# Kernel tuning notes

Hardware: AMD Instinct MI355X
Metric: run time of the kernel (lower is better)

Reference implementation:

```python
import jax, jax.numpy as jnp
import numpy as np

B, S, E, H = 4, 2048, 1024, 16
HD = E // H  # 64 head dim


def setup_inputs() -> dict:
    key = jax.random.key(0)
    ks = jax.random.split(key, 6)
    x = jax.random.normal(ks[0], (B, S, E), dtype=jnp.float32)
    mask = jax.random.randint(ks[1], (B, S, S), 0, 2, dtype=jnp.int32)
    # per-head qkv Linear(E -> 3*HD), stacked over heads: weight [H, 3*HD, E]
    lim = 1.0 / np.sqrt(E)
    Wqkv = jax.random.uniform(ks[2], (H, 3 * HD, E), minval=-lim, maxval=lim, dtype=jnp.float32)
    bqkv = jax.random.uniform(ks[3], (H, 3 * HD), minval=-lim, maxval=lim, dtype=jnp.float32)
    Wo = jax.random.uniform(ks[4], (E, E), minval=-lim, maxval=lim, dtype=jnp.float32)
    bo = jax.random.uniform(ks[5], (E,), minval=-lim, maxval=lim, dtype=jnp.float32)
    return {"x": x, "mask": mask, "Wqkv": Wqkv, "bqkv": bqkv, "Wo": Wo, "bo": bo}


def reference(x, mask, Wqkv, bqkv, Wo, bo):
    # fused per-head qkv projection: [B,S,E] x [H,3HD,E] -> [B,H,S,3HD]
    qkv = jnp.einsum('bse,hfe->bhsf', x, Wqkv) + bqkv[None, :, None, :]
    q, k, v = jnp.split(qkv, 3, axis=-1)  # each [B,H,S,HD]
    scale = 1.0 / jnp.sqrt(jnp.float32(HD))
    scores = jnp.einsum('bhqd,bhkd->bhqk', q, k) * scale  # [B,H,S,S]
    # NOTE: original masked_fill sets masked scores to 0.0 (not -inf)
    scores = jnp.where(mask[:, None, :, :] == 1, 0.0, scores)
    attn = jax.nn.softmax(scores, axis=-1)
    ctx = jnp.einsum('bhqk,bhkd->bhqd', attn, v)  # [B,H,S,HD]
    ctx = ctx.transpose(0, 2, 1, 3).reshape(B, S, E)  # concat heads
    return ctx @ Wo.T + bo
```

## Files before the change

kernel.cpp:

```cpp
#include <hip/hip_runtime.h>
#include <stdint.h>

#define B_ 4
#define S_ 2048
#define E_ 1024
#define H_ 16
#define HD_ 64

typedef __attribute__((ext_vector_type(8))) short bf16x8;
typedef __attribute__((ext_vector_type(4))) float f32x4;

__device__ __forceinline__ ushort f2b(float f) {
    union { float f; uint32_t u; } c; c.f = f;
    return (ushort)((c.u + 0x8000u) >> 16);
}

__device__ __forceinline__ void gl2lds16(const ushort* g, const ushort* l) {
    __builtin_amdgcn_global_load_lds(
        (const __attribute__((address_space(1))) unsigned int*)g,
        (__attribute__((address_space(3))) unsigned int*)l,
        16, 0, 0);
}
__device__ __forceinline__ void gl2lds16raw(const void* g, const void* l) {
    __builtin_amdgcn_global_load_lds(
        (const __attribute__((address_space(1))) unsigned int*)g,
        (__attribute__((address_space(3))) unsigned int*)l,
        16, 0, 0);
}

__global__ __launch_bounds__(256) void cvt_bf16(const float* __restrict__ src,
                                                ushort* __restrict__ dst, int n4) {
    int i = blockIdx.x * 256 + threadIdx.x;
    if (i < n4) {
        float4 f = ((const float4*)src)[i];
        ushort4 o;
        o.x = f2b(f.x); o.y = f2b(f.y); o.z = f2b(f.z); o.w = f2b(f.w);
        ((ushort4*)dst)[i] = o;
    }
}

__global__ __launch_bounds__(256) void pack_mask(const int* __restrict__ mask,
                                                 uint32_t* __restrict__ mb) {
    int i = blockIdx.x * 256 + threadIdx.x;
    unsigned long long bal = __ballot(mask[i] == 1);
    int lane = threadIdx.x & 63;
    if (lane < 2) {
        int b = i >> 22, q = (i >> 11) & 2047, c = i & 2047;
        int kt = c >> 6;
        mb[((uint64_t)(b * 32 + kt) * 2048 + q) * 2 + lane] =
            (lane == 0) ? (uint32_t)bal : (uint32_t)(bal >> 32);
    }
}

template <int KD>
__device__ __forceinline__ void gemm_bt_core(
    const ushort* __restrict__ A, const ushort* __restrict__ Bm,
    int m0, int n0, ushort* As, ushort* Bs, f32x4 (&acc)[4][4])
{
    const int tid  = threadIdx.x;
    const int lane = tid & 63;
    const int wave = tid >> 6;
    const int wm = wave >> 1, wn = wave & 1;
    const int fr = lane & 15;
    const int fk = (lane >> 4) * 8;
    const int lrow = lane >> 2;
    const int lk   = (lane & 3) * 8;

    const f32x4 fz = {0.f, 0.f, 0.f, 0.f};
#pragma unroll
    for (int i = 0; i < 4; ++i)
#pragma unroll
        for (int j = 0; j < 4; ++j) acc[i][j] = fz;

    for (int kt = 0; kt < KD / 32; ++kt) {
        const int k0 = kt * 32;
        __syncthreads();
#pragma unroll
        for (int t = 0; t < 2; ++t) {
            const int r0 = t * 64 + wave * 16;
            gl2lds16(&A [(uint64_t)(m0 + r0 + lrow) * KD + k0 + lk], &As[r0 * 32]);
            gl2lds16(&Bm[(uint64_t)(n0 + r0 + lrow) * KD + k0 + lk], &Bs[r0 * 32]);
        }
        __syncthreads();
        bf16x8 af[4], bfr[4];
#pragma unroll
        for (int i = 0; i < 4; ++i)
            af[i] = *(const bf16x8*)&As[(wm * 64 + i * 16 + fr) * 32 + fk];
#pragma unroll
        for (int j = 0; j < 4; ++j)
            bfr[j] = *(const bf16x8*)&Bs[(wn * 64 + j * 16 + fr) * 32 + fk];
#pragma unroll
        for (int i = 0; i < 4; ++i)
#pragma unroll
            for (int j = 0; j < 4; ++j)
                acc[i][j] = __builtin_amdgcn_mfma_f32_16x16x32_bf16(af[i], bfr[j], acc[i][j], 0, 0, 0);
    }
}

__global__ __launch_bounds__(256) void qkv_gemm(
    const ushort* __restrict__ xb, const ushort* __restrict__ wb,
    const float* __restrict__ bqkv,
    ushort* __restrict__ qo, ushort* __restrict__ ko, ushort* __restrict__ vto)
{
    __shared__ ushort As[128 * 32];
    __shared__ ushort Bs[128 * 32];
    f32x4 acc[4][4];
    const int i = blockIdx.x;
    const int c = i & 7, t = i >> 3;
    const int n0 = (c + 8 * (t % 3)) * 128;
    const int m0 = (t / 3) * 128;
    gemm_bt_core<1024>(xb, wb, m0, n0, As, Bs, acc);

    const int lane = threadIdx.x & 63, wave = threadIdx.x >> 6;
    const int wm = wave >> 1, wn = wave & 1;
    const int col = lane & 15, rg = lane >> 4;
#pragma unroll
    for (int j = 0; j < 4; ++j) {
        const int n = n0 + wn * 64 + j * 16 + col;
        const int h = n / 192, f = n % 192;
        const float bias = bqkv[n];
#pragma unroll
        for (int i2 = 0; i2 < 4; ++i2) {
            const int mbase = m0 + wm * 64 + i2 * 16 + rg * 4;
            if (f < 128) {
#pragma unroll
                for (int v = 0; v < 4; ++v) {
                    const int m = mbase + v;
                    const int b = m >> 11, s = m & 2047;
                    const float val = acc[i2][j][v] + bias;
                    if (f < 64) qo[((uint64_t)(b * 16 + h) * 2048 + s) * 64 + f]        = f2b(val * 0.125f);
                    else        ko[((uint64_t)(b * 16 + h) * 2048 + s) * 64 + (f - 64)] = f2b(val);
                }
            } else {
                const int b = mbase >> 11, s = mbase & 2047;
                ushort4 pk;
                pk.x = f2b(acc[i2][j][0] + bias);
                pk.y = f2b(acc[i2][j][1] + bias);
                pk.z = f2b(acc[i2][j][2] + bias);
                pk.w = f2b(acc[i2][j][3] + bias);
                *(ushort4*)&vto[((uint64_t)(b * 16 + h) * 64 + (f - 128)) * 2048 + s] = pk;
            }
        }
    }
}

__global__ __launch_bounds__(256, 3) void attn_kernel(
    const ushort* __restrict__ qa, const ushort* __restrict__ ka,
    const ushort* __restrict__ vta, const uint32_t* __restrict__ mbits,
    ushort* __restrict__ ctxo)
{
    __shared__ __align__(16) ushort SMEM[128 * 64];
    __shared__ __align__(16) ushort Ks[2][64 * 64];
    __shared__ __align__(16) ushort Vts[2][64 * 64];
    __shared__ __align__(16) uint32_t Ms[2][256];

    const int bid = blockIdx.x;
    const int qb = bid & 15;
    const int bh = bid >> 4;
    const int b = bh >> 4;
    const int tid = threadIdx.x, lane = tid & 63, wave = tid >> 6;
    const int col = lane & 15, rg = lane >> 4;

    const uint64_t bhoff = (uint64_t)bh * (S_ * 64);
    const ushort* qp = qa + bhoff + (uint64_t)qb * 128 * 64;
    const ushort* kp = ka + bhoff;
    const ushort* vp = vta + bhoff;
    const uint32_t* mkb = mbits + ((uint64_t)(b * 32) * 2048 + qb * 128) * 2;

#pragma unroll
    for (int t4 = 0; t4 < 4; ++t4) {
        const int o = (wave * 4 + t4) * 512;
        gl2lds16(&qp[o + lane * 8], &SMEM[o]);
    }
#pragma unroll
    for (int t = 0; t < 2; ++t) {
        const int o = (wave * 2 + t) * 512;
        gl2lds16(&kp[o + lane * 8], &Ks[0][o]);
        const int r0 = (wave * 2 + t) * 8;
        gl2lds16(&vp[(uint64_t)(r0 + (lane >> 3)) * S_ + (lane & 7) * 8], &Vts[0][r0 * 64]);
    }
    if (wave == 0) gl2lds16raw(mkb + lane * 4, &Ms[0][0]);
    __syncthreads();

    bf16x8 aq[2][2];
#pragma unroll
    for (int i = 0; i < 2; ++i)
#pragma unroll
        for (int k2 = 0; k2 < 2; ++k2)
            aq[i][k2] = *(const bf16x8*)&SMEM[(wave * 32 + i * 16 + col) * 64 + k2 * 32 + rg * 8];

    const f32x4 fz = {0.f, 0.f, 0.f, 0.f};
    f32x4 acc[4][2];
#pragma unroll
    for (int dt = 0; dt < 4; ++dt)
#pragma unroll
        for (int i = 0; i < 2; ++i) acc[dt][i] = fz;
    float lsum[2] = {0.f, 0.f};

    ushort* Ps = &SMEM[wave * 2048];

    for (int kt = 0; kt < 32; ++kt) {
        const int buf = kt & 1;
        if (kt < 31) {
            const uint64_t knext = (uint64_t)(kt + 1) * 4096;
#pragma unroll
            for (int t = 0; t < 2; ++t) {
                const int o = (wave * 2 + t) * 512;
                gl2lds16(&kp[knext + o + lane * 8], &Ks[buf ^ 1][o]);
                const int r0 = (wave * 2 + t) * 8;
                gl2lds16(&vp[(uint64_t)(r0 + (lane >> 3)) * S_ + (kt + 1) * 64 + (lane & 7) * 8],
                         &Vts[buf ^ 1][r0 * 64]);
            }
            if (wave == 0) gl2lds16raw(mkb + (uint64_t)(kt + 1) * 4096 + lane * 4,
                                       &Ms[buf ^ 1][0]);
        }

        f32x4 sc[2][4];
#pragma unroll
        for (int j = 0; j < 4; ++j) {
            bf16x8 bk0 = *(const bf16x8*)&Ks[buf][(j * 16 + col) * 64 + rg * 8];
            bf16x8 bk1 = *(const bf16x8*)&Ks[buf][(j * 16 + col) * 64 + 32 + rg * 8];
#pragma unroll
            for (int i = 0; i < 2; ++i) {
                f32x4 z = __builtin_amdgcn_mfma_f32_16x16x32_bf16(bk0, aq[i][0], fz, 0, 0, 0);
                sc[i][j] = __builtin_amdgcn_mfma_f32_16x16x32_bf16(bk1, aq[i][1], z, 0, 0, 0);
            }
        }

#pragma unroll
        for (int i = 0; i < 2; ++i) {
            const int qrow = i * 16 + col;
            const uint2 mw = *(const uint2*)&Ms[buf][(wave * 32 + qrow) * 2];
            float ts = 0.f;
#pragma unroll
            for (int j = 0; j < 4; ++j) {
                const uint32_t w = (j & 2) ? mw.y : mw.x;
                const int base = (j & 1) * 16 + rg * 4;
                ushort4 pk;
                {
                    const float s0 = ((w >> (base + 0)) & 1u) ? 0.f : sc[i][j][0];
                    const float s1 = ((w >> (base + 1)) & 1u) ? 0.f : sc[i][j][1];
                    const float s2 = ((w >> (base + 2)) & 1u) ? 0.f : sc[i][j][2];
                    const float s3 = ((w >> (base + 3)) & 1u) ? 0.f : sc[i][j][3];
                    const float p0 = __expf(s0), p1 = __expf(s1);
                    const float p2 = __expf(s2), p3 = __expf(s3);
                    ts += (p0 + p1) + (p2 + p3);
                    pk.x = f2b(p0); pk.y = f2b(p1); pk.z = f2b(p2); pk.w = f2b(p3);
                }
                const int u = ((j * 2 + (rg >> 1)) ^ (col & 7));
                *(ushort4*)&Ps[qrow * 64 + u * 8 + (rg & 1) * 4] = pk;
            }
            lsum[i] += ts;
        }

        bf16x8 bp[2][2];
#pragma unroll
        for (int i = 0; i < 2; ++i)
#pragma unroll
            for (int k2 = 0; k2 < 2; ++k2)
                bp[i][k2] = *(const bf16x8*)&Ps[(i * 16 + col) * 64 + (((k2 * 4 + rg) ^ (col & 7)) << 3)];
#pragma unroll
        for (int dt = 0; dt < 4; ++dt) {
            bf16x8 av0 = *(const bf16x8*)&Vts[buf][(dt * 16 + col) * 64 + rg * 8];
            bf16x8 av1 = *(const bf16x8*)&Vts[buf][(dt * 16 + col) * 64 + 32 + rg * 8];
#pragma unroll
            for (int i = 0; i < 2; ++i) {
                acc[dt][i] = __builtin_amdgcn_mfma_f32_16x16x32_bf16(av0, bp[i][0], acc[dt][i], 0, 0, 0);
                acc[dt][i] = __builtin_amdgcn_mfma_f32_16x16x32_bf16(av1, bp[i][1], acc[dt][i], 0, 0, 0);
            }
        }
        __syncthreads();
    }

    float linv[2];
#pragma unroll
    for (int i = 0; i < 2; ++i) {
        float ts = lsum[i];
        ts += __shfl_xor(ts, 16);
        ts += __shfl_xor(ts, 32);
        linv[i] = 1.0f / ts;
    }

#pragma unroll
    for (int dt = 0; dt < 4; ++dt)
#pragma unroll
        for (int i = 0; i < 2; ++i) {
            const int q = wave * 32 + i * 16 + col;
            const int d = dt * 16 + rg * 4;
            const int gg = (d >> 3) ^ (q & 7);
            ushort4 pk;
            pk.x = f2b(acc[dt][i][0] * linv[i]);
            pk.y = f2b(acc[dt][i][1] * linv[i]);
            pk.z = f2b(acc[dt][i][2] * linv[i]);
            pk.w = f2b(acc[dt][i][3] * linv[i]);
            *(ushort4*)&SMEM[q * 64 + gg * 8 + (d & 7)] = pk;
        }
    __syncthreads();
    const int h = bh & 15;
    const uint64_t obase = (uint64_t)(b * S_ + qb * 128) * E_ + (uint64_t)h * 64;
#pragma unroll
    for (int t4 = 0; t4 < 4; ++t4) {
        const int id = tid + t4 * 256;
        const int r = id >> 3, c8 = id & 7;
        *(bf16x8*)&ctxo[obase + (uint64_t)r * E_ + c8 * 8] =
            *(const bf16x8*)&SMEM[r * 64 + ((c8 ^ (r & 7)) << 3)];
    }
}

__global__ __launch_bounds__(256) void out_gemm(
    const ushort* __restrict__ ctxb, const ushort* __restrict__ wob,
    const float* __restrict__ bo, float* __restrict__ out)
{
    __shared__ ushort As[128 * 32];
    __shared__ ushort Bs[128 * 32];
    f32x4 acc[4][4];
    const int i = blockIdx.x;
    const int n0 = (i & 7) * 128;
    const int m0 = (i >> 3) * 128;
    gemm_bt_core<1024>(ctxb, wob, m0, n0, As, Bs, acc);

    const int lane = threadIdx.x & 63, wave = threadIdx.x >> 6;
    const int wm = wave >> 1, wn = wave & 1;
    const int col = lane & 15, rg = lane >> 4;
#pragma unroll
    for (int j = 0; j < 4; ++j) {
        const int n = n0 + wn * 64 + j * 16 + col;
        const float bias = bo[n];
#pragma unroll
        for (int i2 = 0; i2 < 4; ++i2) {
            const int mb2 = m0 + wm * 64 + i2 * 16 + rg * 4;
#pragma unroll
            for (int v = 0; v < 4; ++v)
                out[(uint64_t)(mb2 + v) * 1024 + n] = acc[i2][j][v] + bias;
        }
    }
}

extern "C" void kernel_launch(void* const* d_in, const int* in_sizes, int n_in,
                              void* d_out, int out_size, void* d_ws, size_t ws_size,
                              hipStream_t stream)
{
    const float* x    = (const float*)d_in[0];
    const int*   mask = (const int*)d_in[1];
    const float* Wqkv = (const float*)d_in[2];
    const float* bqkv = (const float*)d_in[3];
    const float* Wo   = (const float*)d_in[4];
    const float* bo   = (const float*)d_in[5];
    float* out = (float*)d_out;

    char* p = (char*)d_ws;
    ushort* xb  = (ushort*)p; p += (size_t)8388608 * 2;
    ushort* wqb = (ushort*)p; p += (size_t)3145728 * 2;
    ushort* wob = (ushort*)p; p += (size_t)1048576 * 2;
    ushort* qo  = (ushort*)p; p += (size_t)8388608 * 2;
    ushort* ko  = (ushort*)p; p += (size_t)8388608 * 2;
    ushort* vto = (ushort*)p; p += (size_t)8388608 * 2;
    ushort* ctx = (ushort*)p; p += (size_t)8388608 * 2;
    uint32_t* mb = (uint32_t*)p;

    cvt_bf16<<<8192, 256, 0, stream>>>(x, xb, 2097152);
    cvt_bf16<<<3072, 256, 0, stream>>>(Wqkv, wqb, 786432);
    cvt_bf16<<<1024, 256, 0, stream>>>(Wo, wob, 262144);
    pack_mask<<<65536, 256, 0, stream>>>(mask, mb);
    qkv_gemm<<<1536, 256, 0, stream>>>(xb, wqb, bqkv, qo, ko, vto);
    attn_kernel<<<1024, 256, 0, stream>>>(qo, ko, vto, mb, ctx);
    out_gemm<<<512, 256, 0, stream>>>(ctx, wob, bo, out);
}
```

Baseline: 405.1 us.

## Keep softmax P in registers via permuted K/V LDS layout; change GEMM grid order

The attention kernel now loads K rows into LDS in a permuted order and with an XOR swizzle on K and V tiles. This lets each lane's score MFMA output line up with the B-operand layout of the PV MFMA, so the exponentiated probabilities are packed straight into registers instead of going through an LDS write and read. It also swaps the two GEMMs to a 2D grid with M-major block order. That changes L2 reuse of weight versus activation tiles and could hurt locality compared with the previous grouped ordering.

```diff
diff --git a/kernel.cpp b/kernel.cpp
--- a/kernel.cpp
+++ b/kernel.cpp
@@ -105,10 +105,8 @@
     __shared__ ushort As[128 * 32];
     __shared__ ushort Bs[128 * 32];
     f32x4 acc[4][4];
-    const int i = blockIdx.x;
-    const int c = i & 7, t = i >> 3;
-    const int n0 = (c + 8 * (t % 3)) * 128;
-    const int m0 = (t / 3) * 128;
+    const int m0 = blockIdx.x * 128;
+    const int n0 = blockIdx.y * 128;
     gemm_bt_core<1024>(xb, wb, m0, n0, As, Bs, acc);
 
     const int lane = threadIdx.x & 63, wave = threadIdx.x >> 6;
@@ -167,18 +165,28 @@
     const ushort* vp = vta + bhoff;
     const uint32_t* mkb = mbits + ((uint64_t)(b * 32) * 2048 + qb * 128) * 2;
 
+    const int lr = lane >> 3;
+    const int usw = (lane & 7) ^ lr;
+    const int r0s = wave * 16 + lr;
+    const int r1s = r0s + 8;
+    const int sg0 = (r0s & 32) | ((r0s & 12) << 1) | ((r0s & 16) >> 2) | (r0s & 3);
+    const int sg1 = (r1s & 32) | ((r1s & 12) << 1) | ((r1s & 16) >> 2) | (r1s & 3);
+    const int kb0 = sg0 * 64 + usw * 8;
+    const int kb1 = sg1 * 64 + usw * 8;
+    const int vb0 = r0s * 2048 + usw * 8;
+    const int vb1 = r1s * 2048 + usw * 8;
+    const int ldst0 = wave * 1024;
+    const int ldst1 = ldst0 + 512;
+
 #pragma unroll
     for (int t4 = 0; t4 < 4; ++t4) {
         const int o = (wave * 4 + t4) * 512;
         gl2lds16(&qp[o + lane * 8], &SMEM[o]);
     }
-#pragma unroll
-    for (int t = 0; t < 2; ++t) {
-        const int o = (wave * 2 + t) * 512;
-        gl2lds16(&kp[o + lane * 8], &Ks[0][o]);
-        const int r0 = (wave * 2 + t) * 8;
-        gl2lds16(&vp[(uint64_t)(r0 + (lane >> 3)) * S_ + (lane & 7) * 8], &Vts[0][r0 * 64]);
-    }
+    gl2lds16(&kp[kb0], &Ks[0][ldst0]);
+    gl2lds16(&kp[kb1], &Ks[0][ldst1]);
+    gl2lds16(&vp[vb0], &Vts[0][ldst0]);
+    gl2lds16(&vp[vb1], &Vts[0][ldst1]);
     if (wave == 0) gl2lds16raw(mkb + lane * 4, &Ms[0][0]);
     __syncthreads();
 
@@ -197,20 +205,16 @@
         for (int i = 0; i < 2; ++i) acc[dt][i] = fz;
     float lsum[2] = {0.f, 0.f};
 
-    ushort* Ps = &SMEM[wave * 2048];
+    const int u0 = (rg ^ (col & 7)) << 3;
 
     for (int kt = 0; kt < 32; ++kt) {
         const int buf = kt & 1;
         if (kt < 31) {
-            const uint64_t knext = (uint64_t)(kt + 1) * 4096;
-#pragma unroll
-            for (int t = 0; t < 2; ++t) {
-                const int o = (wave * 2 + t) * 512;
-                gl2lds16(&kp[knext + o + lane * 8], &Ks[buf ^ 1][o]);
-                const int r0 = (wave * 2 + t) * 8;
-                gl2lds16(&vp[(uint64_t)(r0 + (lane >> 3)) * S_ + (kt + 1) * 64 + (lane & 7) * 8],
-                         &Vts[buf ^ 1][r0 * 64]);
-            }
+            const int knext = (kt + 1) * 4096;
+            gl2lds16(&kp[knext + kb0], &Ks[buf ^ 1][ldst0]);
+            gl2lds16(&kp[knext + kb1], &Ks[buf ^ 1][ldst1]);
+            gl2lds16(&vp[vb0 + (kt + 1) * 64], &Vts[buf ^ 1][ldst0]);
+            gl2lds16(&vp[vb1 + (kt + 1) * 64], &Vts[buf ^ 1][ldst1]);
             if (wave == 0) gl2lds16raw(mkb + (uint64_t)(kt + 1) * 4096 + lane * 4,
                                        &Ms[buf ^ 1][0]);
         }
@@ -218,8 +222,8 @@
         f32x4 sc[2][4];
 #pragma unroll
         for (int j = 0; j < 4; ++j) {
-            bf16x8 bk0 = *(const bf16x8*)&Ks[buf][(j * 16 + col) * 64 + rg * 8];
-            bf16x8 bk1 = *(const bf16x8*)&Ks[buf][(j * 16 + col) * 64 + 32 + rg * 8];
+            bf16x8 bk0 = *(const bf16x8*)&Ks[buf][(j * 16 + col) * 64 + u0];
+            bf16x8 bk1 = *(const bf16x8*)&Ks[buf][(j * 16 + col) * 64 + (u0 ^ 32)];
 #pragma unroll
             for (int i = 0; i < 2; ++i) {
                 f32x4 z = __builtin_amdgcn_mfma_f32_16x16x32_bf16(bk0, aq[i][0], fz, 0, 0, 0);
@@ -227,42 +231,35 @@
             }
         }
 
+        bf16x8 bp[2][2];
 #pragma unroll
         for (int i = 0; i < 2; ++i) {
-            const int qrow = i * 16 + col;
-            const uint2 mw = *(const uint2*)&Ms[buf][(wave * 32 + qrow) * 2];
+            const uint2 mw = *(const uint2*)&Ms[buf][(wave * 32 + i * 16 + col) * 2];
             float ts = 0.f;
+            union { ushort u[8]; bf16x8 v; } p0, p1;
 #pragma unroll
             for (int j = 0; j < 4; ++j) {
                 const uint32_t w = (j & 2) ? mw.y : mw.x;
-                const int base = (j & 1) * 16 + rg * 4;
-                ushort4 pk;
-                {
-                    const float s0 = ((w >> (base + 0)) & 1u) ? 0.f : sc[i][j][0];
-                    const float s1 = ((w >> (base + 1)) & 1u) ? 0.f : sc[i][j][1];
-                    const float s2 = ((w >> (base + 2)) & 1u) ? 0.f : sc[i][j][2];
-                    const float s3 = ((w >> (base + 3)) & 1u) ? 0.f : sc[i][j][3];
-                    const float p0 = __expf(s0), p1 = __expf(s1);
-                    const float p2 = __expf(s2), p3 = __expf(s3);
-                    ts += (p0 + p1) + (p2 + p3);
-                    pk.x = f2b(p0); pk.y = f2b(p1); pk.z = f2b(p2); pk.w = f2b(p3);
+                const int sb = rg * 8 + (j & 1) * 4;
+#pragma unroll
+                for (int v = 0; v < 4; ++v) {
+                    const float s = ((w >> (sb + v)) & 1u) ? 0.f : sc[i][j][v];
+                    const float pe = __expf(s);
+                    ts += pe;
+                    const ushort pb = f2b(pe);
+                    if (j < 2) p0.u[(j & 1) * 4 + v] = pb;
+                    else       p1.u[(j & 1) * 4 + v] = pb;
                 }
-                const int u = ((j * 2 + (rg >> 1)) ^ (col & 7));
-                *(ushort4*)&Ps[qrow * 64 + u * 8 + (rg & 1) * 4] = pk;
             }
+            bp[i][0] = p0.v;
+            bp[i][1] = p1.v;
             lsum[i] += ts;
         }
 
-        bf16x8 bp[2][2];
-#pragma unroll
-        for (int i = 0; i < 2; ++i)
-#pragma unroll
-            for (int k2 = 0; k2 < 2; ++k2)
-                bp[i][k2] = *(const bf16x8*)&Ps[(i * 16 + col) * 64 + (((k2 * 4 + rg) ^ (col & 7)) << 3)];
 #pragma unroll
         for (int dt = 0; dt < 4; ++dt) {
-            bf16x8 av0 = *(const bf16x8*)&Vts[buf][(dt * 16 + col) * 64 + rg * 8];
-            bf16x8 av1 = *(const bf16x8*)&Vts[buf][(dt * 16 + col) * 64 + 32 + rg * 8];
+            bf16x8 av0 = *(const bf16x8*)&Vts[buf][(dt * 16 + col) * 64 + u0];
+            bf16x8 av1 = *(const bf16x8*)&Vts[buf][(dt * 16 + col) * 64 + (u0 ^ 32)];
 #pragma unroll
             for (int i = 0; i < 2; ++i) {
                 acc[dt][i] = __builtin_amdgcn_mfma_f32_16x16x32_bf16(av0, bp[i][0], acc[dt][i], 0, 0, 0);
@@ -314,9 +311,8 @@
     __shared__ ushort As[128 * 32];
     __shared__ ushort Bs[128 * 32];
     f32x4 acc[4][4];
-    const int i = blockIdx.x;
-    const int n0 = (i & 7) * 128;
-    const int m0 = (i >> 3) * 128;
+    const int m0 = blockIdx.x * 128;
+    const int n0 = blockIdx.y * 128;
     gemm_bt_core<1024>(ctxb, wob, m0, n0, As, Bs, acc);
 
     const int lane = threadIdx.x & 63, wave = threadIdx.x >> 6;
@@ -362,7 +358,7 @@
     cvt_bf16<<<3072, 256, 0, stream>>>(Wqkv, wqb, 786432);
     cvt_bf16<<<1024, 256, 0, stream>>>(Wo, wob, 262144);
     pack_mask<<<65536, 256, 0, stream>>>(mask, mb);
-    qkv_gemm<<<1536, 256, 0, stream>>>(xb, wqb, bqkv, qo, ko, vto);
+    qkv_gemm<<<dim3(64, 24), 256, 0, stream>>>(xb, wqb, bqkv, qo, ko, vto);
     attn_kernel<<<1024, 256, 0, stream>>>(qo, ko, vto, mb, ctx);
-    out_gemm<<<512, 256, 0, stream>>>(ctx, wob, bo, out);
-}
+    out_gemm<<<dim3(64, 8), 256, 0, stream>>>(ctx, wob, bo, out);
+}
```

Measured after the change: 378.5 us. 1.07x faster.
